# Kernel tuning notes

Hardware: AMD Instinct MI355X
Metric: run time of the kernel (lower is better)

Reference implementation:

```python
import jax, jax.numpy as jnp
import numpy as np

B, M, N, R, FD = 128, 64, 64, 8, 128
BN_EPS = 1e-5
GS_EPS = 1e-8


def conv2d(x, w, b):
    # x: [B,C,H,W], w: [O,C,3,3] or [O,C,1,1]
    y = jax.lax.conv_general_dilated(x, w, (1, 1), 'SAME',
                                     dimension_numbers=('NCHW', 'OIHW', 'NCHW'))
    return y + b[None, :, None, None]


def complex_conv(x, wr, br, wi, bi):
    cr = conv2d(x, wr, br)
    ci = conv2d(x, wi, bi)
    return jnp.concatenate([cr - ci, cr + ci], axis=1)


def batchnorm(x, g, b):
    # training-mode BN over (B,H,W)
    mean = x.mean(axis=(0, 2, 3), keepdims=True)
    var = ((x - mean) ** 2).mean(axis=(0, 2, 3), keepdims=True)
    return g[None, :, None, None] * (x - mean) * jax.lax.rsqrt(var + BN_EPS) + b[None, :, None, None]


def gram_schmidt(mat):
    # mat: [B, M, R, 2]; sequential over R (hard data dependency), vectorized over batch
    Rr = mat.shape[2]
    basis = []  # list of (vr, vi), each [B, M]
    for j in range(Rr):
        vr, vi = mat[:, :, j, 0], mat[:, :, j, 1]
        for br_, bi_ in basis:
            dot_real = jnp.sum(vr * br_ + vi * bi_, axis=1, keepdims=True)
            denom = jnp.sum(br_ * br_ + bi_ * bi_, axis=1, keepdims=True) + GS_EPS
            coef = dot_real / denom  # only real part used (as in torch code)
            vr = vr - coef * br_
            vi = vi - coef * bi_
        nrm = jnp.sqrt(jnp.sum(vr * vr + vi * vi, axis=1, keepdims=True) + GS_EPS)
        basis.append((vr / nrm, vi / nrm))
    return jnp.stack([jnp.stack(p, axis=-1) for p in basis], axis=2)  # [B,M,R,2]


def setup_inputs() -> dict:
    key = jax.random.key(0)
    ks = jax.random.split(key, 32)
    def p(i, shape, fan_in):
        return jax.random.normal(ks[i], shape, jnp.float32) / np.sqrt(fan_in)
    inp = {
        'x':   jax.random.normal(ks[0], (B, M, N, 2), jnp.float32),
        'w1r': p(1, (32, 2, 3, 3), 2 * 9),   'b1r': jnp.zeros((32,), jnp.float32),
        'w1i': p(2, (32, 2, 3, 3), 2 * 9),   'b1i': jnp.zeros((32,), jnp.float32),
        'g1':  jnp.ones((64,), jnp.float32), 'be1': jnp.zeros((64,), jnp.float32),
        'w2r': p(3, (64, 64, 3, 3), 64 * 9), 'b2r': jnp.zeros((64,), jnp.float32),
        'w2i': p(4, (64, 64, 3, 3), 64 * 9), 'b2i': jnp.zeros((64,), jnp.float32),
        'g2':  jnp.ones((128,), jnp.float32), 'be2': jnp.zeros((128,), jnp.float32),
        'w3r': p(5, (FD, 128, 3, 3), 128 * 9), 'b3r': jnp.zeros((FD,), jnp.float32),
        'w3i': p(6, (FD, 128, 3, 3), 128 * 9), 'b3i': jnp.zeros((FD,), jnp.float32),
        'g3':  jnp.ones((2 * FD,), jnp.float32), 'be3': jnp.zeros((2 * FD,), jnp.float32),
        'wu':  p(7, (2 * R, 2 * FD), 2 * FD), 'bu': jnp.zeros((2 * R,), jnp.float32),
        'ws':  p(8, (R, 2 * FD), 2 * FD),     'bs': jnp.zeros((R,), jnp.float32),
        'wv':  p(9, (2 * R, 2 * FD), 2 * FD), 'bv': jnp.zeros((2 * R,), jnp.float32),
    }
    return inp


def forward(x, w1r, b1r, w1i, b1i, g1, be1, w2r, b2r, w2i, b2i, g2, be2,
            w3r, b3r, w3i, b3i, g3, be3, wu, bu, ws, bs, wv, bv):
    h = jnp.transpose(x, (0, 3, 1, 2))  # [B,2,M,N]
    h = jax.nn.relu(batchnorm(complex_conv(h, w1r, b1r, w1i, b1i), g1, be1))
    h = jax.nn.relu(batchnorm(complex_conv(h, w2r, b2r, w2i, b2i), g2, be2))
    h = jax.nn.relu(batchnorm(complex_conv(h, w3r, b3r, w3i, b3i), g3, be3))  # [B,2FD,M,N]
    # u branch: avg over W, 1x1 conv (= channel matmul), relu
    pu = h.mean(axis=3)                                      # [B,2FD,M]
    u = jax.nn.relu(jnp.einsum('bcm,oc->bom', pu, wu) + bu[None, :, None])  # [B,2R,M]
    u = jnp.transpose(u, (0, 2, 1)).reshape(-1, M, R, 2)     # channel c = 2j+part
    u = gram_schmidt(u)
    # s branch: global avg pool + linear + relu
    ps = h.mean(axis=(2, 3))                                 # [B,2FD]
    s = jax.nn.relu(ps @ ws.T + bs)                          # [B,R]
    # v branch: avg over H, 1x1 conv, relu
    pv = h.mean(axis=2)                                      # [B,2FD,N]
    v = jax.nn.relu(jnp.einsum('bcn,oc->bon', pv, wv) + bv[None, :, None])  # [B,2R,N]
    v = jnp.transpose(v, (0, 2, 1)).reshape(-1, N, R, 2)
    v = gram_schmidt(v)
    return (u, s, v)


def reference(x, w1r, b1r, w1i, b1i, g1, be1, w2r, b2r, w2i, b2i, g2, be2,
              w3r, b3r, w3i, b3i, g3, be3, wu, bu, ws, bs, wv, bv):
    return forward(x, w1r, b1r, w1i, b1i, g1, be1, w2r, b2r, w2i, b2i, g2, be2,
                   w3r, b3r, w3i, b3i, g3, be3, wu, bu, ws, bs, wv, bv)
```

## Files before the change

kernel.cpp:

```cpp
#include <hip/hip_runtime.h>

typedef _Float16 f16;
typedef __attribute__((ext_vector_type(8))) short short8;
typedef __attribute__((ext_vector_type(8))) _Float16 half8;
typedef __attribute__((ext_vector_type(4))) float f32x4;

#define DEV __device__ __forceinline__

DEV float h2f(short s) { f16 h; __builtin_memcpy(&h, &s, 2); return (float)h; }
DEV short f2h(float f) { f16 h = (f16)f; short s; __builtin_memcpy(&s, &h, 2); return s; }
DEV half8 s2h8(short8 s) { half8 h; __builtin_memcpy(&h, &s, 16); return h; }

DEV float wave_sum(float v) {
    #pragma unroll
    for (int m = 1; m < 64; m <<= 1) v += __shfl_xor(v, m);
    return v;
}

__global__ __launch_bounds__(256) void prep_w_k(
    const float* __restrict__ wr, const float* __restrict__ wi,
    f16* __restrict__ wf, int CIN, int COUT)
{
    int idx = blockIdx.x * 256 + threadIdx.x;
    int KC = CIN >> 5, NG = (2 * COUT) >> 4;
    int total = 9 * KC * NG * 512;
    if (idx >= total) return;
    int j = idx & 7, lane = (idx >> 3) & 63;
    int t9 = idx >> 9;
    int gg = t9 % NG, s = t9 / NG;
    int tap = s % 9, kc = s / 9;
    int n = gg * 16 + (lane & 15);
    int cin = kc * 32 + (lane >> 4) * 8 + j;
    int o = n < COUT ? n : n - COUT;
    float sgn = n < COUT ? -1.f : 1.f;
    float wv = wr[(o * CIN + cin) * 9 + tap] + sgn * wi[(o * CIN + cin) * 9 + tap];
    wf[idx] = (f16)wv;
}

__global__ __launch_bounds__(256) void conv1_k(
    const float* __restrict__ x,
    const float* __restrict__ w1r, const float* __restrict__ w1i,
    f16* __restrict__ out)
{
    int idx = blockIdx.x * 256 + threadIdx.x;
    int b = idx >> 12, p = idx & 4095;
    int m = p >> 6, n = p & 63;

    float v[2][9];
    #pragma unroll
    for (int dy = 0; dy < 3; ++dy)
        #pragma unroll
        for (int dx = 0; dx < 3; ++dx) {
            int yy = m + dy - 1, xx = n + dx - 1;
            bool ok = (yy >= 0 && yy < 64 && xx >= 0 && xx < 64);
            int base = ((b * 64 + (ok ? yy : 0)) * 64 + (ok ? xx : 0)) * 2;
            v[0][dy*3+dx] = ok ? x[base]     : 0.f;
            v[1][dy*3+dx] = ok ? x[base + 1] : 0.f;
        }

    float o1[64];
    #pragma unroll
    for (int o = 0; o < 32; ++o) {
        float cr = 0.f, ci = 0.f;
        #pragma unroll
        for (int c = 0; c < 2; ++c)
            #pragma unroll
            for (int k = 0; k < 9; ++k) {
                cr = fmaf(v[c][k], w1r[(o*2+c)*9 + k], cr);
                ci = fmaf(v[c][k], w1i[(o*2+c)*9 + k], ci);
            }
        o1[o]      = cr - ci;
        o1[32 + o] = cr + ci;
    }
    f16* ob = out + (size_t)idx * 64;
    #pragma unroll
    for (int grp = 0; grp < 8; ++grp) {
        short8 pk;
        #pragma unroll
        for (int k = 0; k < 8; ++k) pk[k] = f2h(o1[grp*8 + k]);
        *(short8*)(ob + grp * 8) = pk;
    }
}

template<int C8>
__global__ __launch_bounds__(256) void statsv_k(
    const f16* __restrict__ t, float* __restrict__ stats, int iters)
{
    const int C = C8 * 8;
    __shared__ float ls[2 * C];
    const int tid = threadIdx.x;
    const int cg = tid & (C8 - 1), pg = tid / C8;
    const int NG = 256 / C8;
    for (int u = tid; u < 2 * C; u += 256) ls[u] = 0.f;
    __syncthreads();
    float s8[8] = {0,0,0,0,0,0,0,0}, q8[8] = {0,0,0,0,0,0,0,0};
    size_t base = (size_t)blockIdx.x * NG * iters + pg;
    for (int i = 0; i < iters; ++i) {
        size_t pp = base + (size_t)i * NG;
        short8 r = *(const short8*)(t + pp * C + cg * 8);
        #pragma unroll
        for (int k = 0; k < 8; ++k) { float v = h2f(r[k]); s8[k] += v; q8[k] += v * v; }
    }
    #pragma unroll
    for (int k = 0; k < 8; ++k) {
        atomicAdd(&ls[cg*8 + k], s8[k]);
        atomicAdd(&ls[C + cg*8 + k], q8[k]);
    }
    __syncthreads();
    for (int u = tid; u < C; u += 256) {
        atomicAdd(&stats[u], ls[u]);
        atomicAdd(&stats[C + u], ls[C + u]);
    }
}

__global__ void bnparam_k(const float* __restrict__ stats,
                          const float* __restrict__ g, const float* __restrict__ be,
                          float* __restrict__ sc, int C)
{
    int c = threadIdx.x;
    if (c >= C) return;
    const float invN = 1.f / (128.f * 4096.f);
    float mean  = stats[c] * invN;
    float var   = stats[C + c] * invN - mean * mean;
    float scale = g[c] * rsqrtf(var + 1e-5f);
    sc[c]     = scale;
    sc[C + c] = be[c] - mean * scale;
}

template<int CIN, bool CHUNK>
__global__ __launch_bounds__(512, 2) void conv_mfma_k(
    const f16* __restrict__ in, const f16* __restrict__ wf,
    const float* __restrict__ scin, f16* __restrict__ outp,
    float* __restrict__ stats, int n0, int NG, int statsC, int ostride)
{
    constexpr int KQ = CIN / 32;
    constexpr int NSTEP = KQ * 9;
    constexpr int NH   = CHUNK ? 1 : 2;
    constexpr int RW   = 8 / NH;
    constexpr int ROWS = 2 * RW;
    constexpr int SROWS = ROWS + 2;
    constexpr int YT   = 64 / ROWS;
    __shared__ char actl[SROWS*66*32*2];
    __shared__ float lsts[8][64], lstq[8][64];
    const int flat = blockIdx.x;
    const int swzb = (flat & 7) * (128*YT/8) + (flat >> 3);
    const int b = swzb / YT, y0 = (swzb % YT) * ROWS;
    const int tid = threadIdx.x, l = tid & 63, w = tid >> 6;
    const int rp = w / NH, nh = w % NH;
    const int li = l & 15, g = l >> 4;

    f32x4 acc[8][4];
    #pragma unroll
    for (int mf = 0; mf < 8; ++mf)
        #pragma unroll
        for (int nf = 0; nf < 4; ++nf)
            acc[mf][nf] = f32x4{0.f, 0.f, 0.f, 0.f};

    int swz[3];
    #pragma unroll
    for (int dx = 0; dx < 3; ++dx) swz[dx] = ((li + dx) & 7) << 4;

    const f16* wblk = wf + ((size_t)((n0 >> 4) + nh*4) << 9) + (l << 3);
    auto bload = [&](int st, short8* dst) {
        const f16* p = wblk + ((size_t)(st * NG) << 9);
        #pragma unroll
        for (int nf = 0; nf < 4; ++nf) dst[nf] = *(const short8*)(p + (nf << 9));
    };
    short8 breg[4], nbreg[4];
    bload(0, breg);

    for (int st = 0; st < NSTEP; ++st) {
        const int kq = st / 9, tap = st - kq * 9;
        if (tap == 0) {
            half8 scl8, shf8;
            {
                int cb = kq*32 + (tid & 3) * 8;
                #pragma unroll
                for (int k = 0; k < 8; ++k) {
                    scl8[k] = (f16)scin[cb + k];
                    shf8[k] = (f16)scin[CIN + cb + k];
                }
            }
            __syncthreads();
            #pragma unroll
            for (int i = 0; i < (SROWS*66*4 + 511)/512; ++i) {
                int u = tid + i * 512;
                if (u < SROWS*66*4) {
                    int r = u / 264, rem = u - r * 264;
                    int sx = rem >> 2, cg = rem & 3;
                    int srow = y0 - 1 + r, gx = sx - 1;
                    short8 pk = {0,0,0,0,0,0,0,0};
                    if (srow >= 0 && srow < 64 && gx >= 0 && gx < 64) {
                        short8 raw = *(const short8*)(in +
                            ((size_t)(b*4096 + srow*64 + gx)) * CIN + kq*32 + cg*8);
                        half8 rv = s2h8(raw) * scl8 + shf8;
                        short8 sr; __builtin_memcpy(&sr, &rv, 16);
                        pk = sr & ~(sr >> 15);
                    }
                    int off = ((r*66 + sx)*32 + cg*8)*2 ^ ((sx & 7) << 4);
                    *(short8*)(actl + off) = pk;
                }
            }
            __syncthreads();
        }
        if (st + 1 < NSTEP) bload(st + 1, nbreg);
        int dy = (tap * 11) >> 5, dx = tap - dy * 3;
        half8 a[8];
        #pragma unroll
        for (int mf = 0; mf < 8; ++mf) {
            int r = 2*rp + (mf >> 2) + dy;
            int sx = (mf & 3)*16 + li + dx;
            a[mf] = s2h8(*(const short8*)(actl + ((((r*66 + sx)*32) + g*8)*2 ^ swz[dx])));
        }
        __builtin_amdgcn_s_setprio(1);
        #pragma unroll
        for (int mf = 0; mf < 8; ++mf)
            #pragma unroll
            for (int nf = 0; nf < 4; ++nf)
                acc[mf][nf] = __builtin_amdgcn_mfma_f32_16x16x32_f16(a[mf], s2h8(breg[nf]), acc[mf][nf], 0, 0, 0);
        __builtin_amdgcn_s_setprio(0);
        #pragma unroll
        for (int nf = 0; nf < 4; ++nf) breg[nf] = nbreg[nf];
    }

    #pragma unroll
    for (int nf = 0; nf < 4; ++nf) {
        float s = 0.f, q = 0.f;
        #pragma unroll
        for (int mf = 0; mf < 8; ++mf)
            #pragma unroll
            for (int reg = 0; reg < 4; ++reg) {
                float v = acc[mf][nf][reg];
                s += v; q += v * v;
            }
        s += __shfl_xor(s, 16); s += __shfl_xor(s, 32);
        q += __shfl_xor(q, 16); q += __shfl_xor(q, 32);
        if (l < 16) { lsts[w][nf*16 + l] = s; lstq[w][nf*16 + l] = q; }
    }
    __syncthreads();
    if (tid < NH*64) {
        int ch64 = tid & 63, half = tid >> 6;
        float s = 0.f, q = 0.f;
        #pragma unroll
        for (int j = 0; j < RW; ++j) {
            s += lsts[j*NH + half][ch64];
            q += lstq[j*NH + half][ch64];
        }
        atomicAdd(&stats[tid], s);
        atomicAdd(&stats[statsC + tid], q);
    }

    const int obase = nh * 64;
    #pragma unroll
    for (int mf = 0; mf < 8; ++mf) {
        size_t rowbase = (size_t)b * 4096 + (size_t)(y0 + 2*rp + (mf >> 2)) * 64;
        #pragma unroll
        for (int nf = 0; nf < 4; ++nf) {
            int n = obase + nf*16 + li;
            #pragma unroll
            for (int reg = 0; reg < 4; ++reg) {
                int xx = (mf & 3)*16 + g*4 + reg;
                outp[(rowbase + xx) * ostride + n] = (f16)acc[mf][nf][reg];
            }
        }
    }
}

__global__ __launch_bounds__(256) void pool_k(
    const f16* __restrict__ t3c, const float* __restrict__ sc3c,
    float* __restrict__ pu, float* __restrict__ pv, int ncb)
{
    const int b = blockIdx.x, yh = blockIdx.y;
    const int t = threadIdx.x, cg = t & 7, xp = t >> 3;
    const int w = t >> 6, lane = t & 63;
    __shared__ float rq[4][16][64];
    float scl[8], shf[8];
    #pragma unroll
    for (int k = 0; k < 8; ++k) { scl[k] = sc3c[cg*8 + k]; shf[k] = sc3c[64 + cg*8 + k]; }
    float colacc[2][8];
    #pragma unroll
    for (int xi = 0; xi < 2; ++xi)
        #pragma unroll
        for (int k = 0; k < 8; ++k) colacc[xi][k] = 0.f;

    for (int yb = 0; yb < 2; ++yb) {
        for (int yy = 0; yy < 16; ++yy) {
            int y = yh*32 + yb*16 + yy;
            float rc[8];
            #pragma unroll
            for (int xi = 0; xi < 2; ++xi) {
                int xx = xp*2 + xi;
                short8 raw = *(const short8*)(t3c +
                    ((size_t)(b*4096 + y*64 + xx)) * 64 + cg*8);
                #pragma unroll
                for (int k = 0; k < 8; ++k) {
                    float v = fmaxf(fmaf(h2f(raw[k]), scl[k], shf[k]), 0.f);
                    colacc[xi][k] += v;
                    rc[k] = xi ? (rc[k] + v) : v;
                }
            }
            #pragma unroll
            for (int k = 0; k < 8; ++k) {
                rc[k] += __shfl_xor(rc[k], 8);
                rc[k] += __shfl_xor(rc[k], 16);
                rc[k] += __shfl_xor(rc[k], 32);
            }
            if (lane < 8) {
                #pragma unroll
                for (int k = 0; k < 8; ++k) rq[w][yy][lane*8 + k] = rc[k];
            }
        }
        __syncthreads();
        for (int u = t; u < 1024; u += 256) {
            int yy = u >> 6, c = u & 63;
            float v = rq[0][yy][c] + rq[1][yy][c] + rq[2][yy][c] + rq[3][yy][c];
            pu[((size_t)b*256 + ncb + c)*64 + (yh*32 + yb*16 + yy)] = v * (1.f/64.f);
        }
        __syncthreads();
    }
    #pragma unroll
    for (int xi = 0; xi < 2; ++xi)
        #pragma unroll
        for (int k = 0; k < 8; ++k)
            atomicAdd(&pv[((size_t)b*256 + ncb + cg*8 + k)*64 + xp*2 + xi],
                      colacc[xi][k] * (1.f/64.f));
}

__global__ __launch_bounds__(256) void headuv_k(
    const float* __restrict__ pool, const float* __restrict__ w,
    const float* __restrict__ bias, float* __restrict__ out)
{
    int b = blockIdx.x;
    int m = threadIdx.x & 63;
    int ob4 = threadIdx.x >> 6;
    float acc[4] = { bias[ob4], bias[ob4+4], bias[ob4+8], bias[ob4+12] };
    const float* pb = pool + (size_t)b * 256 * 64 + m;
    for (int c = 0; c < 256; ++c) {
        float v = pb[c * 64];
        #pragma unroll
        for (int i = 0; i < 4; ++i)
            acc[i] = fmaf(v, w[(ob4 + i*4) * 256 + c], acc[i]);
    }
    float* op = out + (size_t)b * 16 * 64 + m;
    #pragma unroll
    for (int i = 0; i < 4; ++i)
        op[(ob4 + i*4) * 64] = fmaxf(acc[i], 0.f);
}

__global__ __launch_bounds__(64) void heads_s_k(
    const float* __restrict__ pu, const float* __restrict__ wS,
    const float* __restrict__ bS, float* __restrict__ out)
{
    int b = blockIdx.x, lane = threadIdx.x;
    __shared__ float ls[256];
    for (int i = 0; i < 4; ++i) {
        const float* p = pu + ((size_t)b*256 + lane*4 + i) * 64;
        float s = 0.f;
        for (int m = 0; m < 64; ++m) s += p[m];
        ls[lane*4 + i] = s * (1.f/64.f);
    }
    __syncthreads();
    float acc[8] = {0,0,0,0,0,0,0,0};
    for (int c = lane; c < 256; c += 64) {
        float v = ls[c];
        #pragma unroll
        for (int o = 0; o < 8; ++o) acc[o] = fmaf(v, wS[o*256 + c], acc[o]);
    }
    #pragma unroll
    for (int o = 0; o < 8; ++o) acc[o] = wave_sum(acc[o]);
    if (lane == 0) {
        #pragma unroll
        for (int o = 0; o < 8; ++o)
            out[b*8 + o] = fmaxf(acc[o] + bS[o], 0.f);
    }
}

__global__ __launch_bounds__(64) void gs_k(
    const float* __restrict__ pre, float* __restrict__ out)
{
    int b = blockIdx.x, lane = threadIdx.x;
    const float* pb = pre + (size_t)b * 16 * 64 + lane;
    float vr[8], vi[8], den[8];
    #pragma unroll
    for (int j = 0; j < 8; ++j) { vr[j] = pb[(2*j)*64]; vi[j] = pb[(2*j+1)*64]; }

    #pragma unroll
    for (int j = 0; j < 8; ++j) {
        #pragma unroll
        for (int k = 0; k < j; ++k) {
            float d = wave_sum(vr[j]*vr[k] + vi[j]*vi[k]);
            float coef = d / den[k];
            vr[j] = fmaf(-coef, vr[k], vr[j]);
            vi[j] = fmaf(-coef, vi[k], vi[j]);
        }
        float n2 = wave_sum(vr[j]*vr[j] + vi[j]*vi[j]);
        float inv = 1.f / sqrtf(n2 + 1e-8f);
        vr[j] *= inv; vi[j] *= inv;
        float nn = wave_sum(vr[j]*vr[j] + vi[j]*vi[j]);
        den[j] = nn + 1e-8f;
    }
    float* ob = out + (size_t)b * 64 * 16 + lane * 16;
    #pragma unroll
    for (int j = 0; j < 8; ++j) { ob[j*2] = vr[j]; ob[j*2+1] = vi[j]; }
}

extern "C" void kernel_launch(void* const* d_in, const int* in_sizes, int n_in,
                              void* d_out, int out_size, void* d_ws, size_t ws_size,
                              hipStream_t stream)
{
    const float* x   = (const float*)d_in[0];
    const float* w1r = (const float*)d_in[1];
    const float* w1i = (const float*)d_in[3];
    const float* g1  = (const float*)d_in[5];
    const float* be1 = (const float*)d_in[6];
    const float* w2r = (const float*)d_in[7];
    const float* w2i = (const float*)d_in[9];
    const float* g2  = (const float*)d_in[11];
    const float* be2 = (const float*)d_in[12];
    const float* w3r = (const float*)d_in[13];
    const float* w3i = (const float*)d_in[15];
    const float* g3  = (const float*)d_in[17];
    const float* be3 = (const float*)d_in[18];
    const float* wu  = (const float*)d_in[19];
    const float* bu  = (const float*)d_in[20];
    const float* wS  = (const float*)d_in[21];
    const float* bS  = (const float*)d_in[22];
    const float* wv  = (const float*)d_in[23];
    const float* bv  = (const float*)d_in[24];
    float* out = (float*)d_out;

    char* ws = (char*)d_ws;
    f16*   t2     = (f16*)  (ws + 0);
    f16*   t1     = (f16*)  (ws + 134217728);
    f16*   t3c    = (f16*)  (ws + 134217728);
    float* upre   = (float*)(ws + 134217728);
    float* vpre   = (float*)(ws + 134742016);
    float* pu     = (float*)(ws + 201326592);
    float* pv     = (float*)(ws + 209715200);
    f16*   wfrag2 = (f16*)  (ws + 218103808);
    f16*   wfrag3 = (f16*)  (ws + 218103808);
    float* stats  = (float*)(ws + 219283456);
    float* scsh   = (float*)(ws + 219287040);
    float* stats1 = stats,  *stats2 = stats + 128;
    float* sc1    = scsh,   *sc2    = scsh  + 128, *sc3c = scsh + 384;

    hipMemsetAsync(stats, 0, 3584, stream);
    hipMemsetAsync(pv, 0, (size_t)128*256*64*4, stream);

    prep_w_k<<<288, 256, 0, stream>>>(w2r, w2i, wfrag2, 64, 64);

    conv1_k<<<2048, 256, 0, stream>>>(x, w1r, w1i, t1);
    statsv_k<8><<<1024, 256, 0, stream>>>(t1, stats1, 16);
    bnparam_k<<<1, 64, 0, stream>>>(stats1, g1, be1, sc1, 64);

    conv_mfma_k<64, false><<<1024, 512, 0, stream>>>(
        t1, wfrag2, sc1, t2, stats2,
        0, 8, 128, 128);
    bnparam_k<<<1, 128, 0, stream>>>(stats2, g2, be2, sc2, 128);

    prep_w_k<<<1152, 256, 0, stream>>>(w3r, w3i, wfrag3, 128, 128);
    for (int nc = 0; nc < 4; ++nc) {
        conv_mfma_k<128, true><<<512, 512, 0, stream>>>(
            t2, wfrag3, sc2, t3c, stats + 384 + nc*128,
            nc*64, 16, 64, 64);
        bnparam_k<<<1, 64, 0, stream>>>(stats + 384 + nc*128, g3 + nc*64, be3 + nc*64, sc3c, 64);
        pool_k<<<dim3(128, 2), 256, 0, stream>>>(t3c, sc3c, pu, pv, nc*64);
    }

    headuv_k<<<128, 256, 0, stream>>>(pu, wu, bu, upre);
    headuv_k<<<128, 256, 0, stream>>>(pv, wv, bv, vpre);
    heads_s_k<<<128, 64, 0, stream>>>(pu, wS, bS, out + 131072);

    gs_k<<<128, 64, 0, stream>>>(upre, out);
    gs_k<<<128, 64, 0, stream>>>(vpre, out + 132096);
}
```

Baseline: 741.7 us.

## Triple-buffer conv weight loads with unrolled taps and fold BN params into pool

Restructures the MFMA conv main loop to iterate over channel chunks with a fully unrolled 9-tap inner loop. Weight fragments are prefetched two steps ahead into a three-slot register ring, replacing the single next-step buffer and register copy. This aims to hide global load latency behind MFMA work. Separately, the layer-3 batchnorm scale/shift is now computed inside pool_k from the raw stats, removing four tiny bnparam_k launches. The cost is extra register pressure from the third weight buffer and some redundant per-thread rsqrt work in pool_k.

```diff
diff --git a/kernel.cpp b/kernel.cpp
--- a/kernel.cpp
+++ b/kernel.cpp
@@ -166,12 +166,12 @@
         #pragma unroll
         for (int nf = 0; nf < 4; ++nf) dst[nf] = *(const short8*)(p + (nf << 9));
     };
-    short8 breg[4], nbreg[4];
-    bload(0, breg);
-
-    for (int st = 0; st < NSTEP; ++st) {
-        const int kq = st / 9, tap = st - kq * 9;
-        if (tap == 0) {
+    short8 B[3][4];
+    bload(0, B[0]);
+    if (NSTEP > 1) bload(1, B[1]);
+
+    for (int kq = 0; kq < KQ; ++kq) {
+        {
             half8 scl8, shf8;
             {
                 int cb = kq*32 + (tid & 3) * 8;
@@ -203,24 +203,26 @@
             }
             __syncthreads();
         }
-        if (st + 1 < NSTEP) bload(st + 1, nbreg);
-        int dy = (tap * 11) >> 5, dx = tap - dy * 3;
-        half8 a[8];
-        #pragma unroll
-        for (int mf = 0; mf < 8; ++mf) {
-            int r = 2*rp + (mf >> 2) + dy;
-            int sx = (mf & 3)*16 + li + dx;
-            a[mf] = s2h8(*(const short8*)(actl + ((((r*66 + sx)*32) + g*8)*2 ^ swz[dx])));
-        }
-        __builtin_amdgcn_s_setprio(1);
-        #pragma unroll
-        for (int mf = 0; mf < 8; ++mf)
-            #pragma unroll
-            for (int nf = 0; nf < 4; ++nf)
-                acc[mf][nf] = __builtin_amdgcn_mfma_f32_16x16x32_f16(a[mf], s2h8(breg[nf]), acc[mf][nf], 0, 0, 0);
-        __builtin_amdgcn_s_setprio(0);
-        #pragma unroll
-        for (int nf = 0; nf < 4; ++nf) breg[nf] = nbreg[nf];
+        #pragma unroll
+        for (int tap = 0; tap < 9; ++tap) {
+            const int st = kq * 9 + tap;
+            if (st + 2 < NSTEP) bload(st + 2, B[(tap + 2) % 3]);
+            const int dy = (tap * 11) >> 5, dx = tap - dy * 3;
+            half8 a[8];
+            #pragma unroll
+            for (int mf = 0; mf < 8; ++mf) {
+                int r = 2*rp + (mf >> 2) + dy;
+                int sx = (mf & 3)*16 + li + dx;
+                a[mf] = s2h8(*(const short8*)(actl + ((((r*66 + sx)*32) + g*8)*2 ^ swz[dx])));
+            }
+            __builtin_amdgcn_s_setprio(1);
+            #pragma unroll
+            for (int mf = 0; mf < 8; ++mf)
+                #pragma unroll
+                for (int nf = 0; nf < 4; ++nf)
+                    acc[mf][nf] = __builtin_amdgcn_mfma_f32_16x16x32_f16(a[mf], s2h8(B[tap % 3][nf]), acc[mf][nf], 0, 0, 0);
+            __builtin_amdgcn_s_setprio(0);
+        }
     }
 
     #pragma unroll
@@ -267,7 +269,8 @@
 }
 
 __global__ __launch_bounds__(256) void pool_k(
-    const f16* __restrict__ t3c, const float* __restrict__ sc3c,
+    const f16* __restrict__ t3c, const float* __restrict__ stc,
+    const float* __restrict__ gc, const float* __restrict__ bec,
     float* __restrict__ pu, float* __restrict__ pv, int ncb)
 {
     const int b = blockIdx.x, yh = blockIdx.y;
@@ -275,8 +278,16 @@
     const int w = t >> 6, lane = t & 63;
     __shared__ float rq[4][16][64];
     float scl[8], shf[8];
-    #pragma unroll
-    for (int k = 0; k < 8; ++k) { scl[k] = sc3c[cg*8 + k]; shf[k] = sc3c[64 + cg*8 + k]; }
+    const float invN = 1.f / (128.f * 4096.f);
+    #pragma unroll
+    for (int k = 0; k < 8; ++k) {
+        int c = cg*8 + k;
+        float mean = stc[c] * invN;
+        float var  = stc[64 + c] * invN - mean * mean;
+        float scale = gc[c] * rsqrtf(var + 1e-5f);
+        scl[k] = scale;
+        shf[k] = bec[c] - mean * scale;
+    }
     float colacc[2][8];
     #pragma unroll
     for (int xi = 0; xi < 2; ++xi)
@@ -442,7 +453,7 @@
     float* stats  = (float*)(ws + 219283456);
     float* scsh   = (float*)(ws + 219287040);
     float* stats1 = stats,  *stats2 = stats + 128;
-    float* sc1    = scsh,   *sc2    = scsh  + 128, *sc3c = scsh + 384;
+    float* sc1    = scsh,   *sc2    = scsh  + 128;
 
     hipMemsetAsync(stats, 0, 3584, stream);
     hipMemsetAsync(pv, 0, (size_t)128*256*64*4, stream);
@@ -463,8 +474,8 @@
         conv_mfma_k<128, true><<<512, 512, 0, stream>>>(
             t2, wfrag3, sc2, t3c, stats + 384 + nc*128,
             nc*64, 16, 64, 64);
-        bnparam_k<<<1, 64, 0, stream>>>(stats + 384 + nc*128, g3 + nc*64, be3 + nc*64, sc3c, 64);
-        pool_k<<<dim3(128, 2), 256, 0, stream>>>(t3c, sc3c, pu, pv, nc*64);
+        pool_k<<<dim3(128, 2), 256, 0, stream>>>(
+            t3c, stats + 384 + nc*128, g3 + nc*64, be3 + nc*64, pu, pv, nc*64);
     }
 
     headuv_k<<<128, 256, 0, stream>>>(pu, wu, bu, upre);
```

Result: slower. 1.267 ms (+70.8%).
